# Kernel tuning notes

Hardware: AMD Instinct MI355X
Metric: run time of the kernel (lower is better)

The kernel has to match this reference:

```python
import jax, jax.numpy as jnp
import numpy as np

NUM_HEADS = 12

def setup_inputs() -> dict:
    key = jax.random.key(0)
    ks = jax.random.split(key, 6)
    B, N, C = 4, 2048, 768
    s = 0.02
    return {
        "x": jax.random.normal(ks[0], (B, N, C), jnp.float32),
        "y": jax.random.normal(ks[1], (B, N, C), jnp.float32),
        "Wq": jax.random.normal(ks[2], (C, C), jnp.float32) * s,
        "Wkv": jax.random.normal(ks[3], (2 * C, C), jnp.float32) * s,
        "tau_param": jnp.asarray(1.0, jnp.float32),
        "Wproj": jax.random.normal(ks[4], (C, C), jnp.float32) * s,
        "bproj": jnp.zeros((C,), jnp.float32),
    }

def reference(x, y, Wq, Wkv, tau_param, Wproj, bproj):
    B, N, C = x.shape
    H = NUM_HEADS
    D = C // H
    scale = D ** -0.5
    # q: [B,H,N,D]
    q = (x @ Wq.T).reshape(B, N, H, D).transpose(0, 2, 1, 3) * scale
    kv = (y @ Wkv.T).reshape(B, N, 2, H, D).transpose(2, 0, 3, 1, 4)
    k, v = kv[0], kv[1]
    tau = jax.nn.softplus(tau_param) + 1e-6
    attn = jnp.einsum("bhnd,bhmd->bhnm", q, k) / tau  # [B,H,N,N]
    attn = jax.nn.softmax(attn, axis=-1)
    out = jnp.einsum("bhnm,bhmd->bhnd", attn, v)  # [B,H,N,D]
    out = out.transpose(0, 2, 1, 3).reshape(B, N, C)
    return out @ Wproj.T + bproj
```

## Files before the change

### kernel.cpp

```cpp
#include <hip/hip_runtime.h>
#include <math.h>

typedef unsigned short u16;
typedef unsigned int u32;
typedef __fp16 fp16x2 __attribute__((ext_vector_type(2)));
typedef _Float16 half8 __attribute__((ext_vector_type(8)));
typedef float f32x4 __attribute__((ext_vector_type(4)));

#define NH   12
#define SEQ  2048
#define CDIM 768

__device__ __forceinline__ u16 f2h(float f) {
  _Float16 h = (_Float16)f;
  return __builtin_bit_cast(u16, h);
}
__device__ __forceinline__ u32 pk2(float a, float b) {
  fp16x2 h = __builtin_amdgcn_cvt_pkrtz(a, b);
  return __builtin_bit_cast(u32, h);
}
__device__ __forceinline__ void dma16(const u16* g, u16* l) {
  __builtin_amdgcn_global_load_lds(
      (const __attribute__((address_space(1))) u32*)g,
      (__attribute__((address_space(3))) u32*)l, 16, 0, 0);
}

__global__ __launch_bounds__(256) void cvt_all(
    const float* __restrict__ x, const float* __restrict__ y,
    const float* __restrict__ Wq, const float* __restrict__ Wkv,
    const float* __restrict__ Wp, const float* __restrict__ taup,
    u16* __restrict__ xh, u16* __restrict__ yh,
    u16* __restrict__ wqh, u16* __restrict__ wkh, u16* __restrict__ wph)
{
  const int bx = blockIdx.x;
  const long idx = (long)bx * 1024 + (long)threadIdx.x * 4;
  const float* in; u16* out; long j; float s = 1.f;
  if (bx < 6144)       { in = x;   out = xh;  j = idx; }
  else if (bx < 12288) { in = y;   out = yh;  j = idx - 6144l * 1024; }
  else if (bx < 12864) {
    float t = *taup;
    float sp = (t > 20.f) ? t : log1pf(expf(t));
    s = (0.125f / (sp + 1e-6f)) * 1.44269504088896340736f;
    in = Wq; out = wqh; j = idx - 12288l * 1024;
  }
  else if (bx < 14016) { in = Wkv; out = wkh; j = idx - 12864l * 1024; }
  else                 { in = Wp;  out = wph; j = idx - 14016l * 1024; }
  float4 f = *(const float4*)(in + j);
  *(uint2*)(out + j) = make_uint2(pk2(f.x * s, f.y * s), pk2(f.z * s, f.w * s));
}

template<int MODE, int BN, int WPB>
__global__ __launch_bounds__(256, WPB) void gemm_k(
    const u16* __restrict__ A0, const u16* __restrict__ A1,
    const u16* __restrict__ B0, const u16* __restrict__ B1,
    u16* __restrict__ oq, u16* __restrict__ ok, u16* __restrict__ ovt,
    float* __restrict__ outf, const float* __restrict__ bias)
{
  constexpr int NT = BN / 32;
  __shared__ __align__(16) u16 As[2][128 * 64];
  __shared__ __align__(16) u16 Bs[2][BN * 64];
  const int tid = threadIdx.x;
  const int wave = tid >> 6, lane = tid & 63;
  const int quad = lane >> 4, l16 = lane & 15;
  const int wr = wave >> 1, wc = wave & 1;
  const int row0 = blockIdx.x * 128;
  const int by = blockIdx.y;

  const u16* A; const u16* Bm; int cb;
  if (MODE == 0) {
    if (by < 6) { A = A0; Bm = B0; cb = by; }
    else        { A = A1; Bm = B1; cb = by - 6; }
  } else {
    A = A0; Bm = B0; cb = by;
  }
  const int col0 = cb * BN;

  const int sub = lane >> 3;
  const int csw = ((lane & 7) ^ sub) * 8;

  f32x4 acc[4][NT] = {};

  auto stage = [&](int k0, int bsel) {
    #pragma unroll
    for (int i = 0; i < 4; i++) {
      int ii = wave * 4 + i;
      dma16(A + (size_t)(row0 + ii * 8 + sub) * 768 + k0 + csw, &As[bsel][ii * 512]);
    }
    #pragma unroll
    for (int i = 0; i < BN / 32; i++) {
      int ii = wave * (BN / 32) + i;
      dma16(Bm + (size_t)(col0 + ii * 8 + sub) * 768 + k0 + csw, &Bs[bsel][ii * 512]);
    }
  };

  stage(0, 0);
  __syncthreads();

  #pragma unroll 1
  for (int t = 0; t < 12; t++) {
    const int cur = t & 1;
    if (t + 1 < 12) stage((t + 1) << 6, cur ^ 1);
    const u16* Asp = As[cur];
    const u16* Bsp = Bs[cur];
    #pragma unroll
    for (int ks = 0; ks < 2; ks++) {
      half8 af[4], bfr[NT];
      #pragma unroll
      for (int mt = 0; mt < 4; mt++)
        af[mt] = *(const half8*)&Asp[(wr * 64 + mt * 16 + l16) * 64 + (((ks * 4 + quad) ^ (l16 & 7)) * 8)];
      #pragma unroll
      for (int nt = 0; nt < NT; nt++)
        bfr[nt] = *(const half8*)&Bsp[(wc * (BN / 2) + nt * 16 + l16) * 64 + (((ks * 4 + quad) ^ (l16 & 7)) * 8)];
      #pragma unroll
      for (int mt = 0; mt < 4; mt++)
        #pragma unroll
        for (int nt = 0; nt < NT; nt++)
          acc[mt][nt] = __builtin_amdgcn_mfma_f32_16x16x32_f16(af[mt], bfr[nt], acc[mt][nt], 0, 0, 0);
    }
    __syncthreads();
  }

  #pragma unroll
  for (int mt = 0; mt < 4; mt++)
  #pragma unroll
  for (int nt = 0; nt < NT; nt++) {
    int gm0 = row0 + wr * 64 + mt * 16 + quad * 4;
    int gn = col0 + wc * (BN / 2) + nt * 16 + l16;
    f32x4 v = acc[mt][nt];
    if (MODE == 0) {
      int b = gm0 >> 11, n0 = gm0 & 2047;
      if (by < 6) {
        int h = gn >> 6, d = gn & 63;
        size_t base = (((size_t)(b * NH + h)) * SEQ + n0) * 64 + d;
        #pragma unroll
        for (int r = 0; r < 4; r++) oq[base + (size_t)r * 64] = f2h(v[r]);
      } else if (gn < CDIM) {
        int h = gn >> 6, d = gn & 63;
        size_t base = (((size_t)(b * NH + h)) * SEQ + n0) * 64 + d;
        #pragma unroll
        for (int r = 0; r < 4; r++) ok[base + (size_t)r * 64] = f2h(v[r]);
      } else {
        int c = gn - CDIM;
        int h = c >> 6, d = c & 63;
        *(uint2*)&ovt[(((size_t)(b * NH + h)) * 64 + d) * SEQ + n0] =
            make_uint2(pk2(v[0], v[1]), pk2(v[2], v[3]));
      }
    } else {
      float bv = bias[gn];
      #pragma unroll
      for (int r = 0; r < 4; r++)
        outf[(size_t)(gm0 + r) * CDIM + gn] = v[r] + bv;
    }
  }
}

__global__ __launch_bounds__(256, 3) void attn_kernel(
    const u16* __restrict__ Q, const u16* __restrict__ Kb,
    const u16* __restrict__ Vtg, u16* __restrict__ Ob)
{
  __shared__ __align__(16) u16 Ks[2][64 * 64];
  __shared__ __align__(16) u16 Vs[2][64 * 64];
  __shared__ __align__(16) u16 Ps[4 * 16 * 64];

  const int bid = (blockIdx.x & 7) * 96 + (blockIdx.x >> 3);
  const int qt = bid & 15;
  const int bh = bid >> 4;
  const int b = bh / NH, h = bh % NH;
  const u16* Qp = Q   + (size_t)bh * SEQ * 64;
  const u16* Kp = Kb  + (size_t)bh * SEQ * 64;
  const u16* Vp = Vtg + (size_t)bh * 64 * SEQ;

  const int tid = threadIdx.x;
  const int wave = tid >> 6, lane = tid & 63;
  const int quad = lane >> 4, l16 = lane & 15;
  const int sub = lane >> 3;
  const int csw = ((lane & 7) ^ sub) * 8;
  u16* Pw = Ps + wave * 16 * 64;

  half8 vone;
  #pragma unroll
  for (int j = 0; j < 8; j++) vone[j] = (_Float16)1.0f;

  half8 qf[2][2];
  #pragma unroll
  for (int mt = 0; mt < 2; mt++)
    #pragma unroll
    for (int ks = 0; ks < 2; ks++)
      qf[mt][ks] = *(const half8*)(Qp + (size_t)(qt * 128 + wave * 32 + mt * 16 + l16) * 64 + ks * 32 + quad * 8);

  f32x4 oacc[2][4] = {};
  f32x4 lacc[2] = {};

  auto stage = [&](int kt, int bsel) {
    #pragma unroll
    for (int i = 0; i < 2; i++) {
      int ii = wave * 2 + i;
      dma16(Kp + (size_t)(kt * 64 + ii * 8 + sub) * 64 + csw, &Ks[bsel][ii * 512]);
      dma16(Vp + (size_t)(ii * 8 + sub) * SEQ + kt * 64 + csw, &Vs[bsel][ii * 512]);
    }
  };

  stage(0, 0);
  __syncthreads();

  #pragma unroll 1
  for (int kt = 0; kt < SEQ / 64; kt++) {
    const int cur = kt & 1;
    if (kt + 1 < SEQ / 64) stage(kt + 1, cur ^ 1);
    const u16* Ksp = Ks[cur];
    const u16* Vsp = Vs[cur];

    f32x4 sacc[2][4] = {};
    __builtin_amdgcn_s_setprio(1);
    #pragma unroll
    for (int ks = 0; ks < 2; ks++) {
      #pragma unroll
      for (int ntk = 0; ntk < 4; ntk++) {
        half8 kf = *(const half8*)&Ksp[(ntk * 16 + l16) * 64 + (((ks * 4 + quad) ^ (l16 & 7)) * 8)];
        #pragma unroll
        for (int mt = 0; mt < 2; mt++)
          sacc[mt][ntk] = __builtin_amdgcn_mfma_f32_16x16x32_f16(kf, qf[mt][ks], sacc[mt][ntk], 0, 0, 0);
      }
    }
    __builtin_amdgcn_s_setprio(0);

    half8 pf[2][2];
    #pragma unroll
    for (int mt = 0; mt < 2; mt++) {
      #pragma unroll
      for (int ntk = 0; ntk < 4; ntk++) {
        float p0 = __builtin_amdgcn_exp2f(sacc[mt][ntk][0]);
        float p1 = __builtin_amdgcn_exp2f(sacc[mt][ntk][1]);
        float p2 = __builtin_amdgcn_exp2f(sacc[mt][ntk][2]);
        float p3 = __builtin_amdgcn_exp2f(sacc[mt][ntk][3]);
        *(uint2*)&Pw[l16 * 64 + (((ntk * 2 + (quad >> 1)) ^ (l16 & 7)) * 8) + (quad & 1) * 4] =
            make_uint2(pk2(p0, p1), pk2(p2, p3));
      }
      pf[mt][0] = *(const half8*)&Pw[l16 * 64 + ((quad ^ (l16 & 7)) * 8)];
      pf[mt][1] = *(const half8*)&Pw[l16 * 64 + (((4 + quad) ^ (l16 & 7)) * 8)];
    }

    __builtin_amdgcn_s_setprio(1);
    #pragma unroll
    for (int ks = 0; ks < 2; ks++) {
      #pragma unroll
      for (int dt = 0; dt < 4; dt++) {
        half8 vf = *(const half8*)&Vsp[(dt * 16 + l16) * 64 + (((ks * 4 + quad) ^ (l16 & 7)) * 8)];
        #pragma unroll
        for (int mt = 0; mt < 2; mt++)
          oacc[mt][dt] = __builtin_amdgcn_mfma_f32_16x16x32_f16(pf[mt][ks], vf, oacc[mt][dt], 0, 0, 0);
      }
      #pragma unroll
      for (int mt = 0; mt < 2; mt++)
        lacc[mt] = __builtin_amdgcn_mfma_f32_16x16x32_f16(pf[mt][ks], vone, lacc[mt], 0, 0, 0);
    }
    __builtin_amdgcn_s_setprio(0);

    __syncthreads();
  }

  #pragma unroll
  for (int mt = 0; mt < 2; mt++) {
    #pragma unroll
    for (int r = 0; r < 4; r++) {
      float inv = 1.0f / lacc[mt][r];
      int n = qt * 128 + wave * 32 + mt * 16 + quad * 4 + r;
      size_t base = ((size_t)b * SEQ + n) * CDIM + h * 64;
      #pragma unroll
      for (int dt = 0; dt < 4; dt++)
        Ob[base + dt * 16 + l16] = f2h(oacc[mt][dt][r] * inv);
    }
  }
}

extern "C" void kernel_launch(void* const* d_in, const int* in_sizes, int n_in,
                              void* d_out, int out_size, void* d_ws, size_t ws_size,
                              hipStream_t stream)
{
  const float* x     = (const float*)d_in[0];
  const float* y     = (const float*)d_in[1];
  const float* Wq    = (const float*)d_in[2];
  const float* Wkv   = (const float*)d_in[3];
  const float* taup  = (const float*)d_in[4];
  const float* Wproj = (const float*)d_in[5];
  const float* bproj = (const float*)d_in[6];
  float* out = (float*)d_out;

  char* ws = (char*)d_ws;
  size_t off = 0;
  auto alloc = [&](size_t bytes) { char* p = ws + off; off += bytes; return p; };
  u16* xh  = (u16*)alloc(8192ull * 768 * 2);
  u16* yh  = (u16*)alloc(8192ull * 768 * 2);
  u16* wqh = (u16*)alloc(768ull * 768 * 2);
  u16* wkh = (u16*)alloc(1536ull * 768 * 2);
  u16* wph = (u16*)alloc(768ull * 768 * 2);
  u16* qb  = (u16*)alloc(8192ull * 768 * 2);
  u16* kb  = (u16*)alloc(8192ull * 768 * 2);
  u16* vtb = (u16*)alloc(8192ull * 768 * 2);
  u16* ao  = (u16*)alloc(8192ull * 768 * 2);

  cvt_all<<<14592, 256, 0, stream>>>(x, y, Wq, Wkv, Wproj, taup,
                                     xh, yh, wqh, wkh, wph);

  gemm_k<0, 128, 2><<<dim3(64, 18), 256, 0, stream>>>(xh, yh, wqh, wkh, qb, kb, vtb, nullptr, nullptr);
  attn_kernel<<<dim3(768), 256, 0, stream>>>(qb, kb, vtb, ao);
  gemm_k<2, 64, 3><<<dim3(64, 12), 256, 0, stream>>>(ao, nullptr, wph, nullptr, nullptr, nullptr, nullptr, out, bproj);
}
```

Before: 223.7 us.

## Split attention work across eight waves with one 16-row query tile each

The attention block grows from 4 to 8 waves (512 threads). Each wave now owns 16 query rows instead of 32, so per-wave accumulators, Q fragments and the K/V DMA staging shrink by half. The intent is more parallelism and latency hiding per block with lower register pressure per wave. The cost is that each K/V tile loaded from LDS is reused over fewer MFMAs per wave, the P scratch buffer doubles, and the block-wide barrier now synchronises more waves.

```diff
diff --git a/kernel.cpp b/kernel.cpp
--- a/kernel.cpp
+++ b/kernel.cpp
@@ -154,13 +154,13 @@
   }
 }
 
-__global__ __launch_bounds__(256, 3) void attn_kernel(
+__global__ __launch_bounds__(512, 6) void attn_kernel(
     const u16* __restrict__ Q, const u16* __restrict__ Kb,
     const u16* __restrict__ Vtg, u16* __restrict__ Ob)
 {
   __shared__ __align__(16) u16 Ks[2][64 * 64];
   __shared__ __align__(16) u16 Vs[2][64 * 64];
-  __shared__ __align__(16) u16 Ps[4 * 16 * 64];
+  __shared__ __align__(16) u16 Ps[8 * 16 * 64];
 
   const int bid = (blockIdx.x & 7) * 96 + (blockIdx.x >> 3);
   const int qt = bid & 15;
@@ -175,29 +175,24 @@
   const int quad = lane >> 4, l16 = lane & 15;
   const int sub = lane >> 3;
   const int csw = ((lane & 7) ^ sub) * 8;
-  u16* Pw = Ps + wave * 16 * 64;
+  u16* Pw = Ps + wave * 1024;
 
   half8 vone;
   #pragma unroll
   for (int j = 0; j < 8; j++) vone[j] = (_Float16)1.0f;
 
-  half8 qf[2][2];
-  #pragma unroll
-  for (int mt = 0; mt < 2; mt++)
-    #pragma unroll
-    for (int ks = 0; ks < 2; ks++)
-      qf[mt][ks] = *(const half8*)(Qp + (size_t)(qt * 128 + wave * 32 + mt * 16 + l16) * 64 + ks * 32 + quad * 8);
-
-  f32x4 oacc[2][4] = {};
-  f32x4 lacc[2] = {};
+  half8 qf[2];
+  #pragma unroll
+  for (int ks = 0; ks < 2; ks++)
+    qf[ks] = *(const half8*)(Qp + (size_t)(qt * 128 + wave * 16 + l16) * 64 + ks * 32 + quad * 8);
+
+  f32x4 oacc[4] = {};
+  f32x4 lacc = {};
 
   auto stage = [&](int kt, int bsel) {
-    #pragma unroll
-    for (int i = 0; i < 2; i++) {
-      int ii = wave * 2 + i;
-      dma16(Kp + (size_t)(kt * 64 + ii * 8 + sub) * 64 + csw, &Ks[bsel][ii * 512]);
-      dma16(Vp + (size_t)(ii * 8 + sub) * SEQ + kt * 64 + csw, &Vs[bsel][ii * 512]);
-    }
+    int ii = wave;
+    dma16(Kp + (size_t)(kt * 64 + ii * 8 + sub) * 64 + csw, &Ks[bsel][ii * 512]);
+    dma16(Vp + (size_t)(ii * 8 + sub) * SEQ + kt * 64 + csw, &Vs[bsel][ii * 512]);
   };
 
   stage(0, 0);
@@ -210,35 +205,30 @@
     const u16* Ksp = Ks[cur];
     const u16* Vsp = Vs[cur];
 
-    f32x4 sacc[2][4] = {};
+    f32x4 sacc[4] = {};
     __builtin_amdgcn_s_setprio(1);
     #pragma unroll
     for (int ks = 0; ks < 2; ks++) {
       #pragma unroll
       for (int ntk = 0; ntk < 4; ntk++) {
         half8 kf = *(const half8*)&Ksp[(ntk * 16 + l16) * 64 + (((ks * 4 + quad) ^ (l16 & 7)) * 8)];
-        #pragma unroll
-        for (int mt = 0; mt < 2; mt++)
-          sacc[mt][ntk] = __builtin_amdgcn_mfma_f32_16x16x32_f16(kf, qf[mt][ks], sacc[mt][ntk], 0, 0, 0);
+        sacc[ntk] = __builtin_amdgcn_mfma_f32_16x16x32_f16(kf, qf[ks], sacc[ntk], 0, 0, 0);
       }
     }
     __builtin_amdgcn_s_setprio(0);
 
-    half8 pf[2][2];
-    #pragma unroll
-    for (int mt = 0; mt < 2; mt++) {
-      #pragma unroll
-      for (int ntk = 0; ntk < 4; ntk++) {
-        float p0 = __builtin_amdgcn_exp2f(sacc[mt][ntk][0]);
-        float p1 = __builtin_amdgcn_exp2f(sacc[mt][ntk][1]);
-        float p2 = __builtin_amdgcn_exp2f(sacc[mt][ntk][2]);
-        float p3 = __builtin_amdgcn_exp2f(sacc[mt][ntk][3]);
-        *(uint2*)&Pw[l16 * 64 + (((ntk * 2 + (quad >> 1)) ^ (l16 & 7)) * 8) + (quad & 1) * 4] =
-            make_uint2(pk2(p0, p1), pk2(p2, p3));
-      }
-      pf[mt][0] = *(const half8*)&Pw[l16 * 64 + ((quad ^ (l16 & 7)) * 8)];
-      pf[mt][1] = *(const half8*)&Pw[l16 * 64 + (((4 + quad) ^ (l16 & 7)) * 8)];
-    }
+    #pragma unroll
+    for (int ntk = 0; ntk < 4; ntk++) {
+      float p0 = __builtin_amdgcn_exp2f(sacc[ntk][0]);
+      float p1 = __builtin_amdgcn_exp2f(sacc[ntk][1]);
+      float p2 = __builtin_amdgcn_exp2f(sacc[ntk][2]);
+      float p3 = __builtin_amdgcn_exp2f(sacc[ntk][3]);
+      *(uint2*)&Pw[l16 * 64 + (((ntk * 2 + (quad >> 1)) ^ (l16 & 7)) * 8) + (quad & 1) * 4] =
+          make_uint2(pk2(p0, p1), pk2(p2, p3));
+    }
+    half8 pf[2];
+    pf[0] = *(const half8*)&Pw[l16 * 64 + ((quad ^ (l16 & 7)) * 8)];
+    pf[1] = *(const half8*)&Pw[l16 * 64 + (((4 + quad) ^ (l16 & 7)) * 8)];
 
     __builtin_amdgcn_s_setprio(1);
     #pragma unroll
@@ -246,13 +236,9 @@
       #pragma unroll
       for (int dt = 0; dt < 4; dt++) {
         half8 vf = *(const half8*)&Vsp[(dt * 16 + l16) * 64 + (((ks * 4 + quad) ^ (l16 & 7)) * 8)];
-        #pragma unroll
-        for (int mt = 0; mt < 2; mt++)
-          oacc[mt][dt] = __builtin_amdgcn_mfma_f32_16x16x32_f16(pf[mt][ks], vf, oacc[mt][dt], 0, 0, 0);
+        oacc[dt] = __builtin_amdgcn_mfma_f32_16x16x32_f16(pf[ks], vf, oacc[dt], 0, 0, 0);
       }
-      #pragma unroll
-      for (int mt = 0; mt < 2; mt++)
-        lacc[mt] = __builtin_amdgcn_mfma_f32_16x16x32_f16(pf[mt][ks], vone, lacc[mt], 0, 0, 0);
+      lacc = __builtin_amdgcn_mfma_f32_16x16x32_f16(pf[ks], vone, lacc, 0, 0, 0);
     }
     __builtin_amdgcn_s_setprio(0);
 
@@ -260,16 +246,13 @@
   }
 
   #pragma unroll
-  for (int mt = 0; mt < 2; mt++) {
-    #pragma unroll
-    for (int r = 0; r < 4; r++) {
-      float inv = 1.0f / lacc[mt][r];
-      int n = qt * 128 + wave * 32 + mt * 16 + quad * 4 + r;
-      size_t base = ((size_t)b * SEQ + n) * CDIM + h * 64;
-      #pragma unroll
-      for (int dt = 0; dt < 4; dt++)
-        Ob[base + dt * 16 + l16] = f2h(oacc[mt][dt][r] * inv);
-    }
+  for (int r = 0; r < 4; r++) {
+    float inv = 1.0f / lacc[r];
+    int n = qt * 128 + wave * 16 + quad * 4 + r;
+    size_t base = ((size_t)b * SEQ + n) * CDIM + h * 64;
+    #pragma unroll
+    for (int dt = 0; dt < 4; dt++)
+      Ob[base + dt * 16 + l16] = f2h(oacc[dt][r] * inv);
   }
 }
 
@@ -303,6 +286,6 @@
                                      xh, yh, wqh, wkh, wph);
 
   gemm_k<0, 128, 2><<<dim3(64, 18), 256, 0, stream>>>(xh, yh, wqh, wkh, qb, kb, vtb, nullptr, nullptr);
-  attn_kernel<<<dim3(768), 256, 0, stream>>>(qb, kb, vtb, ao);
+  attn_kernel<<<dim3(768), 512, 0, stream>>>(qb, kb, vtb, ao);
   gemm_k<2, 64, 3><<<dim3(64, 12), 256, 0, stream>>>(ao, nullptr, wph, nullptr, nullptr, nullptr, nullptr, out, bproj);
 }
```

Result: slower. 232.5 us (+3.9%).

## Split attention key tiles across wave pairs with 512-thread blocks

Applied to the files above, without the earlier changes.

The attention kernel now runs 8 waves per block. Each pair of waves shares the same 32 query rows, and each wave in a pair handles half of every 64-key tile. Partial outputs and row sums are combined through LDS at the end, and the P buffer uses a padded stride instead of an XOR swizzle. The aim is more waves per CU for latency hiding and less per-wave work per tile. The cost is an extra LDS reduction, higher register and occupancy pressure under launch bounds of (512,4), and possible bank conflicts from the new P layout.

```diff
diff --git a/kernel.cpp b/kernel.cpp
--- a/kernel.cpp
+++ b/kernel.cpp
@@ -154,13 +154,11 @@
   }
 }
 
-__global__ __launch_bounds__(256, 3) void attn_kernel(
+__global__ __launch_bounds__(512, 4) void attn_kernel(
     const u16* __restrict__ Q, const u16* __restrict__ Kb,
     const u16* __restrict__ Vtg, u16* __restrict__ Ob)
 {
-  __shared__ __align__(16) u16 Ks[2][64 * 64];
-  __shared__ __align__(16) u16 Vs[2][64 * 64];
-  __shared__ __align__(16) u16 Ps[4 * 16 * 64];
+  __shared__ __align__(16) u16 lds[26624];
 
   const int bid = (blockIdx.x & 7) * 96 + (blockIdx.x >> 3);
   const int qt = bid & 15;
@@ -175,7 +173,10 @@
   const int quad = lane >> 4, l16 = lane & 15;
   const int sub = lane >> 3;
   const int csw = ((lane & 7) ^ sub) * 8;
-  u16* Pw = Ps + wave * 16 * 64;
+  const int pair = wave >> 1;
+  const int kh   = wave & 1;
+  const int koff = kh * 32, koff8 = kh * 4;
+  u16* Pw = &lds[16384] + wave * 1280;
 
   half8 vone;
   #pragma unroll
@@ -186,18 +187,14 @@
   for (int mt = 0; mt < 2; mt++)
     #pragma unroll
     for (int ks = 0; ks < 2; ks++)
-      qf[mt][ks] = *(const half8*)(Qp + (size_t)(qt * 128 + wave * 32 + mt * 16 + l16) * 64 + ks * 32 + quad * 8);
+      qf[mt][ks] = *(const half8*)(Qp + (size_t)(qt * 128 + pair * 32 + mt * 16 + l16) * 64 + ks * 32 + quad * 8);
 
   f32x4 oacc[2][4] = {};
   f32x4 lacc[2] = {};
 
   auto stage = [&](int kt, int bsel) {
-    #pragma unroll
-    for (int i = 0; i < 2; i++) {
-      int ii = wave * 2 + i;
-      dma16(Kp + (size_t)(kt * 64 + ii * 8 + sub) * 64 + csw, &Ks[bsel][ii * 512]);
-      dma16(Vp + (size_t)(ii * 8 + sub) * SEQ + kt * 64 + csw, &Vs[bsel][ii * 512]);
-    }
+    dma16(Kp + (size_t)(kt * 64 + wave * 8 + sub) * 64 + csw, &lds[bsel * 4096 + wave * 512]);
+    dma16(Vp + (size_t)(wave * 8 + sub) * SEQ + kt * 64 + csw, &lds[8192 + bsel * 4096 + wave * 512]);
   };
 
   stage(0, 0);
@@ -207,16 +204,16 @@
   for (int kt = 0; kt < SEQ / 64; kt++) {
     const int cur = kt & 1;
     if (kt + 1 < SEQ / 64) stage(kt + 1, cur ^ 1);
-    const u16* Ksp = Ks[cur];
-    const u16* Vsp = Vs[cur];
-
-    f32x4 sacc[2][4] = {};
+    const u16* Ksp = &lds[cur * 4096];
+    const u16* Vsp = &lds[8192 + cur * 4096];
+
+    f32x4 sacc[2][2] = {};
     __builtin_amdgcn_s_setprio(1);
     #pragma unroll
     for (int ks = 0; ks < 2; ks++) {
       #pragma unroll
-      for (int ntk = 0; ntk < 4; ntk++) {
-        half8 kf = *(const half8*)&Ksp[(ntk * 16 + l16) * 64 + (((ks * 4 + quad) ^ (l16 & 7)) * 8)];
+      for (int ntk = 0; ntk < 2; ntk++) {
+        half8 kf = *(const half8*)&Ksp[(koff + ntk * 16 + l16) * 64 + (((ks * 4 + quad) ^ (l16 & 7)) * 8)];
         #pragma unroll
         for (int mt = 0; mt < 2; mt++)
           sacc[mt][ntk] = __builtin_amdgcn_mfma_f32_16x16x32_f16(kf, qf[mt][ks], sacc[mt][ntk], 0, 0, 0);
@@ -224,51 +221,72 @@
     }
     __builtin_amdgcn_s_setprio(0);
 
-    half8 pf[2][2];
+    half8 pf[2];
     #pragma unroll
     for (int mt = 0; mt < 2; mt++) {
-      #pragma unroll
-      for (int ntk = 0; ntk < 4; ntk++) {
+      u16* Pmt = Pw + mt * 640;
+      #pragma unroll
+      for (int ntk = 0; ntk < 2; ntk++) {
         float p0 = __builtin_amdgcn_exp2f(sacc[mt][ntk][0]);
         float p1 = __builtin_amdgcn_exp2f(sacc[mt][ntk][1]);
         float p2 = __builtin_amdgcn_exp2f(sacc[mt][ntk][2]);
         float p3 = __builtin_amdgcn_exp2f(sacc[mt][ntk][3]);
-        *(uint2*)&Pw[l16 * 64 + (((ntk * 2 + (quad >> 1)) ^ (l16 & 7)) * 8) + (quad & 1) * 4] =
+        *(uint2*)&Pmt[l16 * 40 + (ntk * 2 + (quad >> 1)) * 8 + (quad & 1) * 4] =
             make_uint2(pk2(p0, p1), pk2(p2, p3));
       }
-      pf[mt][0] = *(const half8*)&Pw[l16 * 64 + ((quad ^ (l16 & 7)) * 8)];
-      pf[mt][1] = *(const half8*)&Pw[l16 * 64 + (((4 + quad) ^ (l16 & 7)) * 8)];
+      pf[mt] = *(const half8*)&Pmt[l16 * 40 + quad * 8];
     }
 
     __builtin_amdgcn_s_setprio(1);
     #pragma unroll
-    for (int ks = 0; ks < 2; ks++) {
+    for (int dt = 0; dt < 4; dt++) {
+      half8 vf = *(const half8*)&Vsp[(dt * 16 + l16) * 64 + (((koff8 + quad) ^ (l16 & 7)) * 8)];
+      #pragma unroll
+      for (int mt = 0; mt < 2; mt++)
+        oacc[mt][dt] = __builtin_amdgcn_mfma_f32_16x16x32_f16(pf[mt], vf, oacc[mt][dt], 0, 0, 0);
+    }
+    #pragma unroll
+    for (int mt = 0; mt < 2; mt++)
+      lacc[mt] = __builtin_amdgcn_mfma_f32_16x16x32_f16(pf[mt], vone, lacc[mt], 0, 0, 0);
+    __builtin_amdgcn_s_setprio(0);
+
+    __syncthreads();
+  }
+
+  float* Oex = (float*)lds + pair * 2048;
+  float* Lex = (float*)&lds[16384] + pair * 32;
+  if (kh) {
+    #pragma unroll
+    for (int mt = 0; mt < 2; mt++)
+      #pragma unroll
+      for (int dt = 0; dt < 4; dt++)
+        *(f32x4*)&Oex[(mt * 4 + dt) * 256 + lane * 4] = oacc[mt][dt];
+    if (l16 == 0) {
+      #pragma unroll
+      for (int mt = 0; mt < 2; mt++)
+        #pragma unroll
+        for (int r = 0; r < 4; r++)
+          Lex[mt * 16 + quad * 4 + r] = lacc[mt][r];
+    }
+  }
+  __syncthreads();
+  if (!kh) {
+    #pragma unroll
+    for (int mt = 0; mt < 2; mt++) {
+      float linv[4];
+      #pragma unroll
+      for (int r = 0; r < 4; r++)
+        linv[r] = 1.0f / (lacc[mt][r] + Lex[mt * 16 + quad * 4 + r]);
       #pragma unroll
       for (int dt = 0; dt < 4; dt++) {
-        half8 vf = *(const half8*)&Vsp[(dt * 16 + l16) * 64 + (((ks * 4 + quad) ^ (l16 & 7)) * 8)];
-        #pragma unroll
-        for (int mt = 0; mt < 2; mt++)
-          oacc[mt][dt] = __builtin_amdgcn_mfma_f32_16x16x32_f16(pf[mt][ks], vf, oacc[mt][dt], 0, 0, 0);
+        f32x4 o2 = *(const f32x4*)&Oex[(mt * 4 + dt) * 256 + lane * 4];
+        #pragma unroll
+        for (int r = 0; r < 4; r++) {
+          int n = qt * 128 + pair * 32 + mt * 16 + quad * 4 + r;
+          Ob[((size_t)b * SEQ + n) * CDIM + h * 64 + dt * 16 + l16] =
+              f2h((oacc[mt][dt][r] + o2[r]) * linv[r]);
+        }
       }
-      #pragma unroll
-      for (int mt = 0; mt < 2; mt++)
-        lacc[mt] = __builtin_amdgcn_mfma_f32_16x16x32_f16(pf[mt][ks], vone, lacc[mt], 0, 0, 0);
-    }
-    __builtin_amdgcn_s_setprio(0);
-
-    __syncthreads();
-  }
-
-  #pragma unroll
-  for (int mt = 0; mt < 2; mt++) {
-    #pragma unroll
-    for (int r = 0; r < 4; r++) {
-      float inv = 1.0f / lacc[mt][r];
-      int n = qt * 128 + wave * 32 + mt * 16 + quad * 4 + r;
-      size_t base = ((size_t)b * SEQ + n) * CDIM + h * 64;
-      #pragma unroll
-      for (int dt = 0; dt < 4; dt++)
-        Ob[base + dt * 16 + l16] = f2h(oacc[mt][dt][r] * inv);
     }
   }
 }
@@ -303,6 +321,6 @@
                                      xh, yh, wqh, wkh, wph);
 
   gemm_k<0, 128, 2><<<dim3(64, 18), 256, 0, stream>>>(xh, yh, wqh, wkh, qb, kb, vtb, nullptr, nullptr);
-  attn_kernel<<<dim3(768), 256, 0, stream>>>(qb, kb, vtb, ao);
+  attn_kernel<<<dim3(768), 512, 0, stream>>>(qb, kb, vtb, ao);
   gemm_k<2, 64, 3><<<dim3(64, 12), 256, 0, stream>>>(ao, nullptr, wph, nullptr, nullptr, nullptr, nullptr, out, bproj);
 }
```

Result: slower. 231.8 us (+3.6%).
